# Optimization experiments

Hardware: AMD Instinct MI355X
Metric: run time of the kernel (lower is better)

## Reference

```python
import jax, jax.numpy as jnp
import numpy as np

B = 4      # cfg.TRAIN.IMS_PER_BATCH
P = 256    # proposals per image (equal per image; all labels > 0)
C = 151    # cfg.MODEL.NUM_CLASSES
R = 51     # cfg.MODEL.NUM_RELATIONS
W = 0.5    # cfg.REL_INFER.NONE_BGREL_WEIGHT


def setup_inputs() -> dict:
    key = jax.random.key(0)
    k1, k2, k3, k4 = jax.random.split(key, 4)
    roi_scores = jax.random.normal(k1, (B * P, C), dtype=jnp.float32)
    rel_scores = jax.random.normal(k2, (B * P * P, R), dtype=jnp.float32)
    roi_labels = jax.random.randint(k3, (B * P,), 1, C, dtype=jnp.int32)  # labels > 0 (fg only)
    # sparse relation co-occurrence matrix densified; background relation slice set to 1
    relationship_mat = (jax.random.uniform(k4, (C, C, R)) < 0.05).astype(jnp.float32)
    relationship_mat = relationship_mat.at[:, :, 0].set(1.0)
    return {
        "roi_scores": roi_scores,
        "rel_scores": rel_scores,
        "relationship_mat": relationship_mat,
        "roi_labels": roi_labels,
        "num_images": B,
    }


def reference(roi_scores, rel_scores, relationship_mat, roi_labels, num_images):
    nb = num_images
    p = roi_scores.shape[0] // nb
    rel = rel_scores.reshape(nb, p, p, -1)          # [B, P, P, R]
    labels = roi_labels.reshape(nb, p)              # [B, P]
    # computed in the original forward but unused by the returned loss
    _unary = jax.nn.log_softmax(roi_scores, axis=1)
    off_diag = (1.0 - jnp.eye(p, dtype=roi_scores.dtype))  # zero out p == q pairs

    def per_image(lab, rl):
        # lab: [P] int, rl: [P, P, R]
        A = relationship_mat[lab]        # [P, C, R]  rows gathered by subject label
        At = relationship_mat[:, lab]    # [C, P, R]  cols gathered by subject label
        # b[p,q,c] = A[p,c,0]*rl[p,q,0] + W * sum_{r>=1} A[p,c,r]*rl[p,q,r]
        b = A[:, None, :, 0] * rl[:, :, None, 0] \
            + W * jnp.einsum('pcr,pqr->pqc', A[..., 1:], rl[..., 1:])
        # t[p,q,c] = At[c,p,0]*rl[q,p,0] + W * sum_{r>=1} At[c,p,r]*rl[q,p,r]
        t = At[..., 0].T[:, None, :] * rl[..., 0].T[:, :, None] \
            + W * jnp.einsum('cpr,qpr->pqc', At[..., 1:], rl[..., 1:])
        theta = 0.5 * (b + t) * off_diag[:, :, None]  # mask diagonal pairs
        theta = theta.sum(0)                          # sum over partner p -> [P, C]
        logp = jax.nn.log_softmax(theta, axis=1)
        return -logp[jnp.arange(p), lab]              # [P]

    loss = jax.vmap(per_image)(labels, rel)           # [B, P]
    return loss.mean()
```

## Files before the change

kernel.cpp:

```cpp
#include <hip/hip_runtime.h>
#include <math.h>

#define NB 4
#define PP 256
#define CC 151
#define RR 51
#define CM 160
#define KS 32
#define NROW (NB*PP)
#define MLB 10240
#define NRELROW (NB*PP*PP)
#define CONVB (NRELROW/8)
#define PREPB (CC*2)

typedef _Float16 half8 __attribute__((ext_vector_type(8)));
typedef _Float16 half2v __attribute__((ext_vector_type(2)));
typedef float floatx16 __attribute__((ext_vector_type(16)));

#define OFF_M1 ((size_t)0)
#define OFF_M2 (OFF_M1 + (size_t)CC*MLB*2)
#define OFF_PT (OFF_M2 + (size_t)CC*MLB*2)
#define OFF_R16 (OFF_PT + (size_t)NROW*KS*CM*4)

__global__ __launch_bounds__(256) void prep_kernel(const float* __restrict__ M,
                                                   const float* __restrict__ rel,
                                                   _Float16* __restrict__ m1,
                                                   _Float16* __restrict__ m2,
                                                   _Float16* __restrict__ rel16,
                                                   float* __restrict__ out) {
    const int bid = blockIdx.x;
    if (bid < PREPB) {
        const int l = (bid < CC) ? bid : bid - CC;
        const int mat = (bid < CC) ? 0 : 1;
        if (bid == 0 && threadIdx.x == 0) *out = 0.f;
        _Float16* dst = (mat ? m2 : m1) + (size_t)l * MLB;
        for (int e = threadIdx.x; e < MLB; e += 256) {
            int oct = e / 1280;
            int rem = e - oct * 1280;
            int c = rem >> 3, j = rem & 7;
            int r = oct * 8 + j;
            float v = 0.f;
            if (r < RR && c < CC) {
                size_t src = ((size_t)(mat ? c * CC + l : l * CC + c)) * RR + r;
                v = (r == 0 ? 0.5f : 0.25f) * M[src];
            }
            dst[e] = (_Float16)v;
        }
    } else {
        const int t = threadIdx.x;
        const size_t row = (size_t)(bid - PREPB) * 8 + (t >> 5);
        const int d  = t & 31;
        const int h0 = 2 * d;
        const int a  = ((int)row >> 8) & 255;
        const int b  = (int)row & 255;
        const bool live = (a != b);
        const float* src = rel + row * RR;
        float v0 = (live && h0 < RR)     ? src[h0]     : 0.f;
        float v1 = (live && h0 + 1 < RR) ? src[h0 + 1] : 0.f;
        half2v p;
        p[0] = (_Float16)v0;
        p[1] = (_Float16)v1;
        *(half2v*)(rel16 + row * 64 + h0) = p;
    }
}

__global__ __launch_bounds__(256) void gemm_kernel(const _Float16* __restrict__ rel16,
                                                   const _Float16* __restrict__ m1,
                                                   const _Float16* __restrict__ m2,
                                                   const int* __restrict__ labels,
                                                   float* __restrict__ part) {
    __shared__ _Float16 Bt[6][2560];
    const int tid  = threadIdx.x;
    const int ks   = blockIdx.x & 31;
    const int rbk  = (blockIdx.x >> 5) & 1;
    const int n    = blockIdx.x >> 6;
    const int wave = tid >> 6, lane = tid & 63;
    const int m32  = lane & 31, kh = lane >> 5;
    const int i0   = ks * 8;
    const int rowimg = rbk * 128 + wave * 32 + m32;

    int labs[8];
    #pragma unroll
    for (int j = 0; j < 8; ++j) labs[j] = labels[n * PP + i0 + j];

    floatx16 acc[5];
    #pragma unroll
    for (int ct = 0; ct < 5; ++ct)
        #pragma unroll
        for (int r2 = 0; r2 < 16; ++r2) acc[ct][r2] = 0.f;

    half8 aS[4];

    auto stageB = [&](int h, int buf) {
        const int il = h >> 3, mh = (h >> 2) & 1, t = h & 3;
        const _Float16* base = (mh ? m2 : m1) + (size_t)labs[il] * MLB + t * 2560;
        __builtin_amdgcn_global_load_lds(
            (const __attribute__((address_space(1))) unsigned int*)(base + tid * 8),
            (__attribute__((address_space(3))) unsigned int*)(&Bt[buf][tid * 8]),
            16, 0, 0);
        __builtin_amdgcn_global_load_lds(
            (const __attribute__((address_space(1))) unsigned int*)(base + 2048 + tid * 2),
            (__attribute__((address_space(3))) unsigned int*)(&Bt[buf][2048 + tid * 2]),
            4, 0, 0);
    };
    auto loadA = [&](int h) {
        const int il = h >> 3, mh = (h >> 2) & 1, t = h & 3;
        const int i = i0 + il;
        const size_t row = mh ? ((size_t)(n * PP + rowimg) * PP + i)
                              : ((size_t)(n * PP + i) * PP + rowimg);
        aS[h & 3] = *(const half8*)(rel16 + row * 64 + t * 16 + kh * 8);
    };
    auto computeStep = [&](int h) {
        const _Float16* bb = &Bt[h % 6][(size_t)(kh * 160 + m32) * 8];
        #pragma unroll
        for (int ct = 0; ct < 5; ++ct) {
            half8 b = *(const half8*)(bb + ct * 256);
            acc[ct] = __builtin_amdgcn_mfma_f32_32x32x16_f16(aS[h & 3], b, acc[ct], 0, 0, 0);
        }
    };

    stageB(0, 0); loadA(0);
    stageB(1, 1); loadA(1);
    stageB(2, 2); loadA(2);

    #pragma unroll
    for (int h = 0; h < 64; ++h) {
        if (h + 3 < 64) { stageB(h + 3, (h + 3) % 6); loadA(h + 3); }
        if (h <= 60)      asm volatile("s_waitcnt vmcnt(9)" ::: "memory");
        else if (h == 61) asm volatile("s_waitcnt vmcnt(6)" ::: "memory");
        else if (h == 62) asm volatile("s_waitcnt vmcnt(3)" ::: "memory");
        else              asm volatile("s_waitcnt vmcnt(0)" ::: "memory");
        __builtin_amdgcn_s_barrier();
        computeStep(h);
    }

    float* pb = part + ((size_t)(n * PP + rbk * 128 + wave * 32) * KS + ks) * CM;
    #pragma unroll
    for (int ct = 0; ct < 5; ++ct)
        #pragma unroll
        for (int reg = 0; reg < 16; ++reg) {
            int row = (reg & 3) + 8 * (reg >> 2) + 4 * kh;
            pb[(size_t)row * KS * CM + ct * 32 + m32] = acc[ct][reg];
        }
}

__global__ __launch_bounds__(256) void reduce_loss_kernel(const float* __restrict__ part,
                                                          const int* __restrict__ labels,
                                                          float* __restrict__ out) {
    __shared__ float th[CM];
    const int row = blockIdx.x;
    const int t = threadIdx.x;
    if (t < CM) {
        const float* p = part + (size_t)row * KS * CM + t;
        float s = 0.f;
        #pragma unroll
        for (int ks = 0; ks < KS; ++ks)
            s += p[ks * CM];
        th[t] = s;
    }
    __syncthreads();
    if (t < 64) {
        float v0 = (t < CC)       ? th[t]       : -INFINITY;
        float v1 = (t + 64 < CC)  ? th[t + 64]  : -INFINITY;
        float v2 = (t + 128 < CC) ? th[t + 128] : -INFINITY;
        float m = fmaxf(v0, fmaxf(v1, v2));
        #pragma unroll
        for (int o = 32; o > 0; o >>= 1) m = fmaxf(m, __shfl_xor(m, o, 64));
        float s = 0.f;
        if (t < CC)       s += expf(v0 - m);
        if (t + 64 < CC)  s += expf(v1 - m);
        if (t + 128 < CC) s += expf(v2 - m);
        #pragma unroll
        for (int o = 32; o > 0; o >>= 1) s += __shfl_xor(s, o, 64);
        if (t == 0) {
            atomicAdd(out, (m + logf(s) - th[labels[row]]) * (1.0f / NROW));
        }
    }
}

extern "C" void kernel_launch(void* const* d_in, const int* in_sizes, int n_in,
                              void* d_out, int out_size, void* d_ws, size_t ws_size,
                              hipStream_t stream) {
    const float* rel    = (const float*)d_in[1];
    const float* relmat = (const float*)d_in[2];
    const int*   labels = (const int*)d_in[3];
    float* out = (float*)d_out;
    char* ws = (char*)d_ws;

    _Float16* m1    = (_Float16*)(ws + OFF_M1);
    _Float16* m2    = (_Float16*)(ws + OFF_M2);
    float*    part  = (float*)(ws + OFF_PT);
    _Float16* rel16 = (_Float16*)(ws + OFF_R16);

    prep_kernel<<<PREPB + CONVB, 256, 0, stream>>>(relmat, rel, m1, m2, rel16, out);
    gemm_kernel<<<NB * 2 * KS, 256, 0, stream>>>(rel16, m1, m2, labels, part);
    reduce_loss_kernel<<<NROW, 256, 0, stream>>>(part, labels, out);
}
```

Measured before the change: 147.8 us.

## Fuse fp32-to-fp16 relation conversion and diagonal masking into GEMM A loads

The separate prep pass that turned rel_scores into a padded fp16 buffer with the diagonal zeroed is removed. The GEMM now loads fp32 rel rows directly with unaligned float4 loads, zeroes diagonal pairs in registers and converts to fp16 just before the MFMA. This saves a full read and write of the relation tensor plus one extra read. In exchange the GEMM reads twice as many bytes for A through misaligned 16-byte loads. The K padding (r from 51 to 63) now pulls neighbouring row data that is multiplied by the zero-padded B, and the vmcnt wait thresholds are raised to match the extra loads.

After: 159.0 us. 1.08x slower.

```diff
diff --git a/kernel.cpp b/kernel.cpp
--- a/kernel.cpp
+++ b/kernel.cpp
@@ -8,63 +8,42 @@
 #define CM 160
 #define KS 32
 #define NROW (NB*PP)
+#define RELTOT (NB*PP*PP*RR)
 #define MLB 10240
-#define NRELROW (NB*PP*PP)
-#define CONVB (NRELROW/8)
 #define PREPB (CC*2)
 
 typedef _Float16 half8 __attribute__((ext_vector_type(8)));
-typedef _Float16 half2v __attribute__((ext_vector_type(2)));
 typedef float floatx16 __attribute__((ext_vector_type(16)));
+typedef float float4u __attribute__((ext_vector_type(4), aligned(4)));
 
 #define OFF_M1 ((size_t)0)
 #define OFF_M2 (OFF_M1 + (size_t)CC*MLB*2)
 #define OFF_PT (OFF_M2 + (size_t)CC*MLB*2)
-#define OFF_R16 (OFF_PT + (size_t)NROW*KS*CM*4)
 
 __global__ __launch_bounds__(256) void prep_kernel(const float* __restrict__ M,
-                                                   const float* __restrict__ rel,
                                                    _Float16* __restrict__ m1,
                                                    _Float16* __restrict__ m2,
-                                                   _Float16* __restrict__ rel16,
                                                    float* __restrict__ out) {
     const int bid = blockIdx.x;
-    if (bid < PREPB) {
-        const int l = (bid < CC) ? bid : bid - CC;
-        const int mat = (bid < CC) ? 0 : 1;
-        if (bid == 0 && threadIdx.x == 0) *out = 0.f;
-        _Float16* dst = (mat ? m2 : m1) + (size_t)l * MLB;
-        for (int e = threadIdx.x; e < MLB; e += 256) {
-            int oct = e / 1280;
-            int rem = e - oct * 1280;
-            int c = rem >> 3, j = rem & 7;
-            int r = oct * 8 + j;
-            float v = 0.f;
-            if (r < RR && c < CC) {
-                size_t src = ((size_t)(mat ? c * CC + l : l * CC + c)) * RR + r;
-                v = (r == 0 ? 0.5f : 0.25f) * M[src];
-            }
-            dst[e] = (_Float16)v;
+    const int l = (bid < CC) ? bid : bid - CC;
+    const int mat = (bid < CC) ? 0 : 1;
+    if (bid == 0 && threadIdx.x == 0) *out = 0.f;
+    _Float16* dst = (mat ? m2 : m1) + (size_t)l * MLB;
+    for (int e = threadIdx.x; e < MLB; e += 256) {
+        int oct = e / 1280;
+        int rem = e - oct * 1280;
+        int c = rem >> 3, j = rem & 7;
+        int r = oct * 8 + j;
+        float v = 0.f;
+        if (r < RR && c < CC) {
+            size_t src = ((size_t)(mat ? c * CC + l : l * CC + c)) * RR + r;
+            v = (r == 0 ? 0.5f : 0.25f) * M[src];
         }
-    } else {
-        const int t = threadIdx.x;
-        const size_t row = (size_t)(bid - PREPB) * 8 + (t >> 5);
-        const int d  = t & 31;
-        const int h0 = 2 * d;
-        const int a  = ((int)row >> 8) & 255;
-        const int b  = (int)row & 255;
-        const bool live = (a != b);
-        const float* src = rel + row * RR;
-        float v0 = (live && h0 < RR)     ? src[h0]     : 0.f;
-        float v1 = (live && h0 + 1 < RR) ? src[h0 + 1] : 0.f;
-        half2v p;
-        p[0] = (_Float16)v0;
-        p[1] = (_Float16)v1;
-        *(half2v*)(rel16 + row * 64 + h0) = p;
+        dst[e] = (_Float16)v;
     }
 }
 
-__global__ __launch_bounds__(256) void gemm_kernel(const _Float16* __restrict__ rel16,
+__global__ __launch_bounds__(256) void gemm_kernel(const float* __restrict__ rel,
                                                    const _Float16* __restrict__ m1,
                                                    const _Float16* __restrict__ m2,
                                                    const int* __restrict__ labels,
@@ -89,7 +68,7 @@
         #pragma unroll
         for (int r2 = 0; r2 < 16; ++r2) acc[ct][r2] = 0.f;
 
-    half8 aS[4];
+    float4u aF[4][2];
 
     auto stageB = [&](int h, int buf) {
         const int il = h >> 3, mh = (h >> 2) & 1, t = h & 3;
@@ -106,16 +85,28 @@
     auto loadA = [&](int h) {
         const int il = h >> 3, mh = (h >> 2) & 1, t = h & 3;
         const int i = i0 + il;
-        const size_t row = mh ? ((size_t)(n * PP + rowimg) * PP + i)
-                              : ((size_t)(n * PP + i) * PP + rowimg);
-        aS[h & 3] = *(const half8*)(rel16 + row * 64 + t * 16 + kh * 8);
+        const int r0 = t * 16 + kh * 8;
+        int idx = mh ? ((n * PP + rowimg) * PP + i) * RR + r0
+                     : ((n * PP + i) * PP + rowimg) * RR + r0;
+        idx = min(idx, RELTOT - 8);
+        const float* p = rel + idx;
+        aF[h & 3][0] = *(const float4u*)(p);
+        aF[h & 3][1] = *(const float4u*)(p + 4);
     };
     auto computeStep = [&](int h) {
+        const int il = h >> 3;
+        const bool dz = (i0 + il) == rowimg;
+        half8 a;
+        #pragma unroll
+        for (int j = 0; j < 4; ++j) {
+            a[j]     = (_Float16)(dz ? 0.f : aF[h & 3][0][j]);
+            a[j + 4] = (_Float16)(dz ? 0.f : aF[h & 3][1][j]);
+        }
         const _Float16* bb = &Bt[h % 6][(size_t)(kh * 160 + m32) * 8];
         #pragma unroll
         for (int ct = 0; ct < 5; ++ct) {
             half8 b = *(const half8*)(bb + ct * 256);
-            acc[ct] = __builtin_amdgcn_mfma_f32_32x32x16_f16(aS[h & 3], b, acc[ct], 0, 0, 0);
+            acc[ct] = __builtin_amdgcn_mfma_f32_32x32x16_f16(a, b, acc[ct], 0, 0, 0);
         }
     };
 
@@ -126,10 +117,10 @@
     #pragma unroll
     for (int h = 0; h < 64; ++h) {
         if (h + 3 < 64) { stageB(h + 3, (h + 3) % 6); loadA(h + 3); }
-        if (h <= 60)      asm volatile("s_waitcnt vmcnt(9)" ::: "memory");
-        else if (h == 61) asm volatile("s_waitcnt vmcnt(6)" ::: "memory");
-        else if (h == 62) asm volatile("s_waitcnt vmcnt(3)" ::: "memory");
-        else              asm volatile("s_waitcnt vmcnt(0)" ::: "memory");
+        if (h <= 60)      asm volatile("s_waitcnt vmcnt(12)" ::: "memory");
+        else if (h == 61) asm volatile("s_waitcnt vmcnt(8)"  ::: "memory");
+        else if (h == 62) asm volatile("s_waitcnt vmcnt(4)"  ::: "memory");
+        else              asm volatile("s_waitcnt vmcnt(0)"  ::: "memory");
         __builtin_amdgcn_s_barrier();
         computeStep(h);
     }
@@ -190,9 +181,8 @@
     _Float16* m1    = (_Float16*)(ws + OFF_M1);
     _Float16* m2    = (_Float16*)(ws + OFF_M2);
     float*    part  = (float*)(ws + OFF_PT);
-    _Float16* rel16 = (_Float16*)(ws + OFF_R16);
 
-    prep_kernel<<<PREPB + CONVB, 256, 0, stream>>>(relmat, rel, m1, m2, rel16, out);
-    gemm_kernel<<<NB * 2 * KS, 256, 0, stream>>>(rel16, m1, m2, labels, part);
+    prep_kernel<<<PREPB, 256, 0, stream>>>(relmat, m1, m2, out);
+    gemm_kernel<<<NB * 2 * KS, 256, 0, stream>>>(rel, m1, m2, labels, part);
     reduce_loss_kernel<<<NROW, 256, 0, stream>>>(part, labels, out);
 }
```
